# Kernel tuning notes

Hardware: AMD Instinct MI355X
Metric: run time of the kernel (lower is better)

## Reference

```python
import jax, jax.numpy as jnp
import numpy as np

TOP_K = 8
COAL_THR = 0.7

def _sign(x):
    s = jnp.sign(x)
    return jnp.where(s == 0, 1.0, s)

def setup_inputs() -> dict:
    key = jax.random.key(0)
    ks = jax.random.split(key, 12)
    B, N, D, P, H, NC = 4, 4096, 256, 64, 1024, 256
    def lin(k, fi, fo):
        return jax.random.normal(k, (fi, fo), dtype=jnp.float32) / np.sqrt(fi).astype(np.float32)
    return {
        "agent_states": jax.random.normal(ks[0], (B, N, D), dtype=jnp.float32),
        "agent_actions": jax.random.normal(ks[1], (B, N, D), dtype=jnp.float32),
        "episodic_mem": jax.random.normal(ks[2], (B, N, H), dtype=jnp.float32),
        "Wq": lin(ks[3], D, P), "bq": jnp.zeros((P,), jnp.float32),
        "Wk": lin(ks[4], D, P), "bk": jnp.zeros((P,), jnp.float32),
        "Wc": lin(ks[5], D, P), "bc": jnp.zeros((P,), jnp.float32),
        "Wh": lin(ks[6], D, H), "bh": jnp.zeros((H,), jnp.float32),
        "agent_keys": _sign(jax.random.normal(ks[7], (N, H), dtype=jnp.float32)),
        "pos_codes": _sign(jax.random.normal(ks[8], (NC, H), dtype=jnp.float32)),
        "step": 3,
    }

def reference(agent_states, agent_actions, episodic_mem,
              Wq, bq, Wk, bk, Wc, bc, Wh, bh, agent_keys, pos_codes, step):
    B, N, D = agent_states.shape
    P = Wq.shape[1]
    scale = jnp.asarray(np.sqrt(P), agent_states.dtype)

    # --- DynamicGraph.compute_graph(agent_actions) ---
    Q = agent_actions @ Wq + bq                       # (B,N,P)
    K = agent_actions @ Wk + bk                       # (B,N,P)
    scores = jnp.einsum('bnp,bmp->bnm', Q, K) / scale  # (B,N,N)
    _, ti = jax.lax.top_k(scores, TOP_K)               # (B,N,TOP_K)
    flat = scores.reshape(-1, N)
    rows = jnp.arange(flat.shape[0])[:, None]
    mask = jnp.zeros_like(flat).at[rows, ti.reshape(-1, TOP_K)].set(1.0).reshape(scores.shape)
    masked = scores * mask + (1.0 - mask) * (-1e9)
    adjacency = jax.nn.softmax(masked, axis=-1)        # (B,N,N)

    # message passing: each agent perceives a top-k mix of neighbor states
    incoming = jnp.einsum('bnm,bmd->bnd', adjacency, agent_states)  # (B,N,D)

    # --- AgentCombination(incoming, agent_actions) ---
    proj = agent_actions @ Wc + bc                    # (B,N,P)
    pn = proj / jnp.maximum(jnp.linalg.norm(proj, axis=-1, keepdims=True), 1e-12)
    sim = jnp.einsum('bnp,bmp->bnm', pn, pn)           # (B,N,N)
    cmask = (sim > COAL_THR).astype(proj.dtype)
    cw = cmask / (jnp.sum(cmask, axis=-1, keepdims=True) + 1e-8)
    combined = jnp.einsum('bnm,bmd->bnd', cw, incoming)
    out_states = 0.8 * incoming + 0.2 * combined      # (B,N,D)

    # --- HDCMemory: to_hdc -> bind agent key -> write(position) -> read ---
    hdc = jnp.tanh(3.0 * (out_states @ Wh + bh))       # (B,N,H) soft-bipolar
    personal = hdc * agent_keys[None]                  # bind with per-agent key
    pos = pos_codes[step % pos_codes.shape[0]]         # (H,)
    bound = personal * pos                             # bind with position code
    new_episodic = 0.95 * episodic_mem + 0.05 * bound  # write with decay
    # read: torch-style cosine similarity (norms clamped at 1e-8)
    na = jnp.maximum(jnp.linalg.norm(new_episodic, axis=-1), 1e-8)
    nb = jnp.maximum(jnp.linalg.norm(personal, axis=-1), 1e-8)
    mem_sim = jnp.sum(new_episodic * personal, axis=-1) / (na * nb)  # (B,N)

    return out_states, new_episodic, mem_sim
```

## Files before the change

### kernel.cpp

```cpp
#include <hip/hip_runtime.h>

#define BB 4
#define NN 4096
#define DD 256
#define PP 64
#define HH 1024
#define NCC 256
#define TOPK 8
#define CAP2 128

typedef __attribute__((ext_vector_type(8))) short s8v;
typedef __attribute__((ext_vector_type(4))) float f4v;

__device__ __forceinline__ void gload_lds16b(const unsigned short* g, unsigned short* l) {
    __builtin_amdgcn_global_load_lds(
        (const __attribute__((address_space(1))) void*)g,
        (__attribute__((address_space(3))) void*)l, 16, 0, 0);
}
__device__ __forceinline__ unsigned short f2b(float f) {
    unsigned int u = __float_as_uint(f);
    unsigned int r = (u + 0x7FFFu + ((u >> 16) & 1u)) >> 16;
    return (unsigned short)r;
}

__global__ __launch_bounds__(64) void k_gram(const float* __restrict__ Wk,
                                             float* __restrict__ G)
{
    int i = blockIdx.x, j = threadIdx.x;
    float s = 0.f;
#pragma unroll 8
    for (int d = 0; d < DD; ++d)
        s = fmaf(Wk[d * PP + i], Wk[d * PP + j], s);
    G[i * PP + j] = s;
}

__global__ __launch_bounds__(256) void k_proj(
    const float* __restrict__ act,
    const float* __restrict__ Wq, const float* __restrict__ bq,
    const float* __restrict__ Wk, const float* __restrict__ bk,
    const float* __restrict__ Wc, const float* __restrict__ bc,
    const float* __restrict__ Wh, const float* __restrict__ G,
    float* __restrict__ Qo, float* __restrict__ Ko,
    unsigned short* __restrict__ PNb, unsigned short* __restrict__ Whb,
    unsigned short* __restrict__ Kbo, float* __restrict__ Tg)
{
    __shared__ float As[16][DD];
    __shared__ float Ps[16][PP];
    const int tid = threadIdx.x;
    const long row0 = (long)blockIdx.x * 16;

    {
        const float4* g4 = (const float4*)(act + row0 * DD);
        float4* s4 = (float4*)(&As[0][0]);
#pragma unroll
        for (int i = 0; i < 4; ++i) s4[tid + i * 256] = g4[tid + i * 256];
    }
    {
        int h = blockIdx.x;
        Whb[(long)h * DD + tid] = f2b(Wh[(long)tid * HH + h]);
    }
    __syncthreads();

    const int col = tid & 63;
    const int rg  = tid >> 6;
    float aq[4], ak[4], ac[4];
#pragma unroll
    for (int j = 0; j < 4; ++j) { aq[j] = bq[col]; ak[j] = bk[col]; ac[j] = bc[col]; }

    for (int d = 0; d < DD; ++d) {
        float wq = Wq[d * PP + col];
        float wk = Wk[d * PP + col];
        float wc = Wc[d * PP + col];
#pragma unroll
        for (int j = 0; j < 4; ++j) {
            float a = As[rg * 4 + j][d];
            aq[j] = fmaf(a, wq, aq[j]);
            ak[j] = fmaf(a, wk, ak[j]);
            ac[j] = fmaf(a, wc, ac[j]);
        }
    }
    __syncthreads();

#pragma unroll
    for (int j = 0; j < 4; ++j) {
        long r = row0 + rg * 4 + j;
        Qo[r * PP + col] = aq[j];
        Ko[r * PP + col] = ak[j];
        Kbo[r * PP + col] = f2b(ak[j]);
        Ps[rg * 4 + j][col] = ac[j];
        As[rg * 4 + j][col] = aq[j];
    }
    __syncthreads();

    const int w = tid >> 6;
    const int lane = tid & 63;
#pragma unroll
    for (int j = 0; j < 4; ++j) {
        int r = w * 4 + j;
        float v = Ps[r][lane];
        float ss = v * v;
#pragma unroll
        for (int off = 32; off >= 1; off >>= 1) ss += __shfl_xor(ss, off, 64);
        float nrm = fmaxf(sqrtf(ss), 1e-12f);
        PNb[(row0 + r) * PP + lane] = f2b(v / nrm);
    }

#pragma unroll
    for (int j = 0; j < 4; ++j) {
        int r = w * 4 + j;
        float qc = As[r][lane];
        float gq = 0.f;
#pragma unroll 8
        for (int c2 = 0; c2 < 64; ++c2)
            gq = fmaf(G[c2 * PP + lane], As[r][c2], gq);
        float s2 = qc * gq;
        float mu = qc * bk[lane];
#pragma unroll
        for (int off = 32; off >= 1; off >>= 1) {
            s2 += __shfl_xor(s2, off, 64);
            mu += __shfl_xor(mu, off, 64);
        }
        if (lane == 0)
            Tg[row0 + r] = mu + 2.25f * sqrtf(fmaxf(s2, 0.f));
    }
}

__global__ __launch_bounds__(512, 8) void k_topk(
    const float* __restrict__ Q, const float* __restrict__ K,
    const unsigned short* __restrict__ Kb, const float* __restrict__ Tg,
    const float* __restrict__ states, float* __restrict__ incoming)
{
    __shared__ float Qsf[32][64];
    __shared__ unsigned short Bsb[2][128 * 64];
    __shared__ int cnt[32];
    __shared__ unsigned short lst[32][CAP2];
    __shared__ float scr[32][CAP2];

    const int tid = threadIdx.x;
    const int lane = tid & 63;
    const int wid = tid >> 6;
    const int obid = ((blockIdx.x & 7) << 6) | (blockIdx.x >> 3);
    const int b  = obid >> 7;
    const int n0 = (obid & 127) << 5;
    const int r = lane & 15, g = lane >> 4;

    if (tid < 32) cnt[tid] = 0;
    ((float4*)&Qsf[0][0])[tid] = ((const float4*)(Q + ((long)b * NN + n0) * PP))[tid];

    const unsigned short* KbB = Kb + (long)b * NN * PP;
    {
#pragma unroll
        for (int t = 0; t < 2; ++t) {
            int q = t * 512 + tid;
            int row = q >> 3, c = q & 7;
            int cs = c ^ (row & 7);
            gload_lds16b(KbB + row * PP + cs * 8,
                         &Bsb[0][0] + (t * 512 + wid * 64) * 8);
        }
    }
    __syncthreads();

    s8v afr[2][2];
#pragma unroll
    for (int j = 0; j < 2; ++j)
#pragma unroll
        for (int s = 0; s < 2; ++s) {
            int c = s * 4 + g;
            float4 x0 = *(const float4*)(&Qsf[j * 16 + r][c * 8]);
            float4 x1 = *(const float4*)(&Qsf[j * 16 + r][c * 8 + 4]);
            s8v h;
            h[0] = (short)f2b(x0.x); h[1] = (short)f2b(x0.y);
            h[2] = (short)f2b(x0.z); h[3] = (short)f2b(x0.w);
            h[4] = (short)f2b(x1.x); h[5] = (short)f2b(x1.y);
            h[6] = (short)f2b(x1.z); h[7] = (short)f2b(x1.w);
            afr[j][s] = h;
        }
    float tT[2][4];
#pragma unroll
    for (int j = 0; j < 2; ++j)
#pragma unroll
        for (int rr2 = 0; rr2 < 4; ++rr2)
            tT[j][rr2] = Tg[(long)b * NN + n0 + j * 16 + g * 4 + rr2];

    int cur = 0;
    for (int mt = 0; mt < NN / 128; ++mt) {
        if (mt + 1 < NN / 128) {
            const unsigned short* kb = KbB + (long)((mt + 1) << 7) * PP;
#pragma unroll
            for (int t = 0; t < 2; ++t) {
                int q = t * 512 + tid;
                int row = q >> 3, c = q & 7;
                int cs = c ^ (row & 7);
                gload_lds16b(kb + row * PP + cs * 8,
                             &Bsb[cur ^ 1][0] + (t * 512 + wid * 64) * 8);
            }
        }

        {
            const int m0 = mt << 7;
            const int mloc = wid * 16 + r;
            s8v bfr[2];
#pragma unroll
            for (int s = 0; s < 2; ++s) {
                int cd = (s * 4 + g) ^ (mloc & 7);
                bfr[s] = *(const s8v*)(&Bsb[cur][0] + mloc * 64 + cd * 8);
            }
#pragma unroll
            for (int j = 0; j < 2; ++j) {
                f4v acc = {0.f, 0.f, 0.f, 0.f};
#pragma unroll
                for (int s = 0; s < 2; ++s)
                    acc = __builtin_amdgcn_mfma_f32_16x16x32_bf16(afr[j][s], bfr[s], acc, 0, 0, 0);
#pragma unroll
                for (int rr2 = 0; rr2 < 4; ++rr2) {
                    if (acc[rr2] >= tT[j][rr2]) {
                        int qrow = j * 16 + g * 4 + rr2;
                        int pos = atomicAdd(&cnt[qrow], 1);
                        if (pos < CAP2)
                            lst[qrow][pos] = (unsigned short)(m0 + wid * 16 + r);
                    }
                }
            }
        }
        __syncthreads();
        cur ^= 1;
    }

    const int g16 = lane >> 4, li = lane & 15;
    const float4* K4all = (const float4*)(K + (long)b * NN * PP);
    for (int rr = wid * 4; rr < wid * 4 + 4; ++rr) {
        int c = cnt[rr]; if (c > CAP2) c = CAP2;

        float4 q4 = *(const float4*)(&Qsf[rr][li * 4]);
        for (int cd = g16; cd < c; cd += 4) {
            int idx = lst[rr][cd];
            float4 kv = K4all[(long)idx * 16 + li];
            float p = q4.x * kv.x;
            p = fmaf(q4.y, kv.y, p);
            p = fmaf(q4.z, kv.z, p);
            p = fmaf(q4.w, kv.w, p);
            p += __shfl_xor(p, 1, 64); p += __shfl_xor(p, 2, 64);
            p += __shfl_xor(p, 4, 64); p += __shfl_xor(p, 8, 64);
            if (li == 0) scr[rr][cd] = p;
        }

        float sc0 = -1e30f, sc1 = -1e30f;
        int i0 = 0x7FFFFFFF, i1 = 0x7FFFFFFF;
        if (lane < c)      { i0 = lst[rr][lane];      sc0 = scr[rr][lane]; }
        if (lane + 64 < c) { i1 = lst[rr][lane + 64]; sc1 = scr[rr][lane + 64]; }

        float wv[TOPK]; int wi[TOPK];
#pragma unroll
        for (int e = 0; e < TOPK; ++e) {
            bool p0 = (sc0 > sc1) || (sc0 == sc1 && i0 < i1);
            float lv = p0 ? sc0 : sc1;
            int   li2 = p0 ? i0 : i1;
#pragma unroll
            for (int off = 32; off >= 1; off >>= 1) {
                float ov = __shfl_xor(lv, off, 64);
                int   oi = __shfl_xor(li2, off, 64);
                bool tk = (ov > lv) || (ov == lv && oi < li2);
                lv = tk ? ov : lv;
                li2 = tk ? oi : li2;
            }
            wv[e] = lv; wi[e] = li2;
            if (sc0 == lv && i0 == li2)      { sc0 = -1e30f; i0 = 0x7FFFFFFF; }
            else if (sc1 == lv && i1 == li2) { sc1 = -1e30f; i1 = 0x7FFFFFFF; }
        }

        float mx = wv[0] * 0.125f;
        float ex[TOPK]; float Z = 0.f;
#pragma unroll
        for (int e = 0; e < TOPK; ++e) { ex[e] = expf(wv[e] * 0.125f - mx); Z += ex[e]; }
        float invZ = 1.0f / Z;

        float4 a0 = {0.f, 0.f, 0.f, 0.f};
#pragma unroll
        for (int e = 0; e < TOPK; ++e) {
            int gi = wi[e] & (NN - 1);
            float4 sv = ((const float4*)(states + ((long)b * NN + gi) * DD))[lane];
            float we = ex[e] * invZ;
            a0.x = fmaf(we, sv.x, a0.x); a0.y = fmaf(we, sv.y, a0.y);
            a0.z = fmaf(we, sv.z, a0.z); a0.w = fmaf(we, sv.w, a0.w);
        }
        ((float4*)(incoming + ((long)b * NN + n0 + rr) * DD))[lane] = a0;
    }
}

#define CAP 64
__global__ __launch_bounds__(256, 4) void k_coal(
    const unsigned short* __restrict__ PNb, const float* __restrict__ incoming,
    float* __restrict__ outs)
{
    __shared__ unsigned short Asb[16 * 64];
    __shared__ unsigned short Bsb[2][128 * 64];
    __shared__ int cnt[16];
    __shared__ unsigned short lst[16][CAP];

    const int tid = threadIdx.x;
    const int lane = tid & 63;
    const int wid = tid >> 6;
    const int obid = ((blockIdx.x & 7) << 7) | (blockIdx.x >> 3);
    const int b  = obid >> 8;
    const int n0 = (obid & 255) << 4;
    const int r = lane & 15, g = lane >> 4;

    if (tid < 16) cnt[tid] = 0;

    const unsigned short* PnB = PNb + (long)b * NN * PP;
    {
        const unsigned short* ab = PnB + (long)n0 * PP;
        if (tid < 128) {
            int row = tid >> 3, c = tid & 7;
            int cs = c ^ (row & 7);
            gload_lds16b(ab + row * PP + cs * 8, Asb + (wid * 64) * 8);
        }
    }
    {
#pragma unroll
        for (int t = 0; t < 4; ++t) {
            int q = t * 256 + tid;
            int row = q >> 3, c = q & 7;
            int cs = c ^ (row & 7);
            gload_lds16b(PnB + row * PP + cs * 8,
                         &Bsb[0][0] + (t * 256 + wid * 64) * 8);
        }
    }
    __syncthreads();

    s8v afr[2];
#pragma unroll
    for (int s = 0; s < 2; ++s) {
        int c = s * 4 + g;
        int cd = c ^ (r & 7);
        afr[s] = *(const s8v*)(Asb + r * 64 + cd * 8);
    }

    int cur = 0;
    for (int mt = 0; mt < NN / 128; ++mt) {
        if (mt + 1 < NN / 128) {
            const unsigned short* bb = PnB + (long)((mt + 1) << 7) * PP;
#pragma unroll
            for (int t = 0; t < 4; ++t) {
                int q = t * 256 + tid;
                int row = q >> 3, c = q & 7;
                int cs = c ^ (row & 7);
                gload_lds16b(bb + row * PP + cs * 8,
                             &Bsb[cur ^ 1][0] + (t * 256 + wid * 64) * 8);
            }
        }

        const int m0 = mt << 7;
#pragma unroll
        for (int t = 0; t < 2; ++t) {
            const int mrow = (wid * 2 + t) * 16 + r;
            f4v acc = {0.f, 0.f, 0.f, 0.f};
#pragma unroll
            for (int s = 0; s < 2; ++s) {
                int c = s * 4 + g;
                int cd = c ^ (mrow & 7);
                s8v bfr = *(const s8v*)(&Bsb[cur][0] + mrow * 64 + cd * 8);
                acc = __builtin_amdgcn_mfma_f32_16x16x32_bf16(afr[s], bfr, acc, 0, 0, 0);
            }
#pragma unroll
            for (int rr2 = 0; rr2 < 4; ++rr2) {
                if (acc[rr2] > 0.7f) {
                    int qrow = g * 4 + rr2;
                    int m = m0 + (wid * 2 + t) * 16 + r;
                    int pos = atomicAdd(&cnt[qrow], 1);
                    if (pos < CAP) lst[qrow][pos] = (unsigned short)m;
                }
            }
        }
        __syncthreads();
        cur ^= 1;
    }

    const int w = tid >> 6;
    for (int rr = w * 4; rr < w * 4 + 4; ++rr) {
        int c = cnt[rr];
        float inv = 1.0f / ((float)c + 1e-8f);
        int cc = (c < CAP) ? c : CAP;
        float ax = 0.f, ay = 0.f, az = 0.f, aw = 0.f;
        for (int i = 0; i < cc; ++i) {
            const float4* ip = (const float4*)(incoming + ((long)b * NN + lst[rr][i]) * DD);
            float4 v = ip[lane];
            ax += v.x; ay += v.y; az += v.z; aw += v.w;
        }
        const float4* self4 = (const float4*)(incoming + ((long)b * NN + n0 + rr) * DD);
        float4 sv = self4[lane];
        float4 o;
        o.x = 0.8f * sv.x + 0.2f * inv * ax;
        o.y = 0.8f * sv.y + 0.2f * inv * ay;
        o.z = 0.8f * sv.z + 0.2f * inv * az;
        o.w = 0.8f * sv.w + 0.2f * inv * aw;
        ((float4*)(outs + ((long)b * NN + n0 + rr) * DD))[lane] = o;
    }
}

__global__ __launch_bounds__(512, 4) void k_mem(
    const float* __restrict__ outs, const unsigned short* __restrict__ Whb,
    const float* __restrict__ bh, const float* __restrict__ keys,
    const float* __restrict__ pos_codes, const int* __restrict__ stepp,
    const float* __restrict__ mem,
    float* __restrict__ epi_out, float* __restrict__ sim_out)
{
    __shared__ unsigned short Ab[32 * 256];
    __shared__ unsigned short Bb[256 * 64];
    __shared__ float red[8][32][3];

    const int tid = threadIdx.x;
    const int lane = tid & 63;
    const int wid = tid >> 6;
    const long row0 = (long)blockIdx.x * 32;
    const int r = lane & 15, g = lane >> 4;

#pragma unroll
    for (int it = 0; it < 2; ++it) {
        int q = it * 512 + tid;
        int row = q >> 5, c = q & 31;
        const float4* src = (const float4*)(outs + (row0 + row) * DD + c * 8);
        float4 x0 = src[0], x1 = src[1];
        s8v h8;
        h8[0] = (short)f2b(x0.x); h8[1] = (short)f2b(x0.y);
        h8[2] = (short)f2b(x0.z); h8[3] = (short)f2b(x0.w);
        h8[4] = (short)f2b(x1.x); h8[5] = (short)f2b(x1.y);
        h8[6] = (short)f2b(x1.z); h8[7] = (short)f2b(x1.w);
        int cd = c ^ (row & 7);
        *(s8v*)(Ab + row * 256 + cd * 8) = h8;
    }

    const int step = stepp[0];
    const int prow = ((step % NCC) + NCC) % NCC;
    float snp[2][4], snn[2][4], spp[2][4];
#pragma unroll
    for (int j = 0; j < 2; ++j)
#pragma unroll
        for (int rr2 = 0; rr2 < 4; ++rr2) { snp[j][rr2] = 0.f; snn[j][rr2] = 0.f; spp[j][rr2] = 0.f; }

    for (int qt = 0; qt < 4; ++qt) {
        f4v acc[2][2];
#pragma unroll
        for (int j = 0; j < 2; ++j)
#pragma unroll
            for (int t = 0; t < 2; ++t) acc[j][t] = (f4v){0.f, 0.f, 0.f, 0.f};

        for (int ks = 0; ks < 4; ++ks) {
            __syncthreads();
            {
#pragma unroll
                for (int t4 = 0; t4 < 4; ++t4) {
                    int q = t4 * 512 + tid;
                    int row = q >> 3, c = q & 7;
                    int cs = c ^ (row & 7);
                    gload_lds16b(Whb + (long)(qt * 256 + row) * DD + ks * 64 + cs * 8,
                                 Bb + (t4 * 512 + wid * 64) * 8);
                }
            }
            __syncthreads();

            s8v af[2][2];
#pragma unroll
            for (int j = 0; j < 2; ++j)
#pragma unroll
                for (int s = 0; s < 2; ++s) {
                    int cA = ks * 8 + s * 4 + g;
                    int rA = j * 16 + r;
                    int cd = cA ^ (rA & 7);
                    af[j][s] = *(const s8v*)(Ab + rA * 256 + cd * 8);
                }
#pragma unroll
            for (int t = 0; t < 2; ++t) {
                const int hloc = (wid * 2 + t) * 16 + r;
#pragma unroll
                for (int s = 0; s < 2; ++s) {
                    int cd = (s * 4 + g) ^ (hloc & 7);
                    s8v bf = *(const s8v*)(Bb + hloc * 64 + cd * 8);
                    acc[0][t] = __builtin_amdgcn_mfma_f32_16x16x32_bf16(af[0][s], bf, acc[0][t], 0, 0, 0);
                    acc[1][t] = __builtin_amdgcn_mfma_f32_16x16x32_bf16(af[1][s], bf, acc[1][t], 0, 0, 0);
                }
            }
        }

#pragma unroll
        for (int t = 0; t < 2; ++t) {
            int h = qt * 256 + (wid * 2 + t) * 16 + r;
            float ps = pos_codes[(long)prow * HH + h];
            float bb_ = bh[h];
#pragma unroll
            for (int j = 0; j < 2; ++j)
#pragma unroll
                for (int rr2 = 0; rr2 < 4; ++rr2) {
                    long row = row0 + j * 16 + g * 4 + rr2;
                    int n = (int)(row & (NN - 1));
                    float y = acc[j][t][rr2] + bb_;
                    float e = __expf(6.0f * y);
                    float hd = 1.0f - __fdividef(2.0f, e + 1.0f);
                    float pe = hd * keys[(long)n * HH + h];
                    float ne = 0.95f * mem[row * HH + h] + 0.05f * (pe * ps);
                    epi_out[row * HH + h] = ne;
                    snp[j][rr2] = fmaf(ne, pe, snp[j][rr2]);
                    snn[j][rr2] = fmaf(ne, ne, snn[j][rr2]);
                    spp[j][rr2] = fmaf(pe, pe, spp[j][rr2]);
                }
        }
    }

#pragma unroll
    for (int j = 0; j < 2; ++j)
#pragma unroll
        for (int rr2 = 0; rr2 < 4; ++rr2) {
#pragma unroll
            for (int off = 1; off <= 8; off <<= 1) {
                snp[j][rr2] += __shfl_xor(snp[j][rr2], off, 64);
                snn[j][rr2] += __shfl_xor(snn[j][rr2], off, 64);
                spp[j][rr2] += __shfl_xor(spp[j][rr2], off, 64);
            }
        }
    if (r == 0) {
#pragma unroll
        for (int j = 0; j < 2; ++j)
#pragma unroll
            for (int rr2 = 0; rr2 < 4; ++rr2) {
                int rw = j * 16 + g * 4 + rr2;
                red[wid][rw][0] = snp[j][rr2];
                red[wid][rw][1] = snn[j][rr2];
                red[wid][rw][2] = spp[j][rr2];
            }
    }
    __syncthreads();
    if (tid < 32) {
        float dot = 0.f, nn = 0.f, pp = 0.f;
#pragma unroll
        for (int wv = 0; wv < 8; ++wv) {
            dot += red[wv][tid][0]; nn += red[wv][tid][1]; pp += red[wv][tid][2];
        }
        float na = fmaxf(sqrtf(nn), 1e-8f);
        float nb = fmaxf(sqrtf(pp), 1e-8f);
        sim_out[row0 + tid] = dot / (na * nb);
    }
}

extern "C" void kernel_launch(void* const* d_in, const int* in_sizes, int n_in,
                              void* d_out, int out_size, void* d_ws, size_t ws_size,
                              hipStream_t stream)
{
    const float* states  = (const float*)d_in[0];
    const float* actions = (const float*)d_in[1];
    const float* mem     = (const float*)d_in[2];
    const float* Wq = (const float*)d_in[3];
    const float* bq = (const float*)d_in[4];
    const float* Wk = (const float*)d_in[5];
    const float* bk = (const float*)d_in[6];
    const float* Wc = (const float*)d_in[7];
    const float* bc = (const float*)d_in[8];
    const float* Wh = (const float*)d_in[9];
    const float* bh = (const float*)d_in[10];
    const float* keys = (const float*)d_in[11];
    const float* pos  = (const float*)d_in[12];
    const int*   step = (const int*)d_in[13];

    float* ws = (float*)d_ws;
    float* Q        = ws;
    float* K        = ws + 1048576;
    unsigned short* PNb = (unsigned short*)(ws + 2097152);
    unsigned short* Whb = PNb + 1048576;
    float* incoming = ws + 3145728;
    unsigned short* Kb = (unsigned short*)(ws + 7340032);
    float* Tg       = ws + 7340032 + 524288;
    float* G        = Tg + 16384;

    float* outs = (float*)d_out;
    float* epi  = outs + (long)BB * NN * DD;
    float* simo = epi + (long)BB * NN * HH;

    hipLaunchKernelGGL(k_gram, dim3(64), dim3(64), 0, stream, Wk, G);
    hipLaunchKernelGGL(k_proj, dim3(BB * NN / 16), dim3(256), 0, stream,
                       actions, Wq, bq, Wk, bk, Wc, bc, Wh, G,
                       Q, K, PNb, Whb, Kb, Tg);
    hipLaunchKernelGGL(k_topk, dim3(BB * (NN / 32)), dim3(512), 0, stream,
                       Q, K, Kb, Tg, states, incoming);
    hipLaunchKernelGGL(k_coal, dim3(BB * (NN / 16)), dim3(256), 0, stream,
                       PNb, incoming, outs);
    hipLaunchKernelGGL(k_mem, dim3(BB * NN / 32), dim3(512), 0, stream,
                       outs, Whb, bh, keys, pos, step, mem, epi, simo);
}
```

Measured before the change: 212.4 us.

## Split top-k kernel into candidate collection and per-row final selection kernels

The fused top-k kernel is split in two. The first kernel does the bf16 MFMA candidate filtering and writes each row's candidate list and count into the incoming buffer as scratch. A second kernel, one wave per row, rescoring candidates in fp32, selects the top-8, applies the softmax and gathers states. The aim is to free LDS in the heavy MFMA kernel for higher occupancy and to spread the serial per-row tail across many small blocks. The cost is an extra launch and a global round trip for the candidate lists.

```diff
diff --git a/kernel.cpp b/kernel.cpp
--- a/kernel.cpp
+++ b/kernel.cpp
@@ -125,16 +125,15 @@
     }
 }
 
-__global__ __launch_bounds__(512, 8) void k_topk(
-    const float* __restrict__ Q, const float* __restrict__ K,
+__global__ __launch_bounds__(512, 8) void k_collect(
+    const float* __restrict__ Q,
     const unsigned short* __restrict__ Kb, const float* __restrict__ Tg,
-    const float* __restrict__ states, float* __restrict__ incoming)
+    float* __restrict__ incoming)
 {
     __shared__ float Qsf[32][64];
     __shared__ unsigned short Bsb[2][128 * 64];
     __shared__ int cnt[32];
     __shared__ unsigned short lst[32][CAP2];
-    __shared__ float scr[32][CAP2];
 
     const int tid = threadIdx.x;
     const int lane = tid & 63;
@@ -195,7 +194,6 @@
                              &Bsb[cur ^ 1][0] + (t * 512 + wid * 64) * 8);
             }
         }
-
         {
             const int m0 = mt << 7;
             const int mloc = wid * 16 + r;
@@ -226,65 +224,87 @@
         cur ^= 1;
     }
 
+    float* ibase = incoming + ((long)b * NN + n0) * DD;
+    if (tid < 32) *(int*)(ibase + (long)tid * DD + 64) = cnt[tid];
+    for (int k = tid; k < 32 * 64; k += 512) {
+        int rr = k >> 6, off = k & 63;
+        ((unsigned int*)(ibase + (long)rr * DD))[off] = ((unsigned int*)&lst[rr][0])[off];
+    }
+}
+
+__global__ __launch_bounds__(256, 8) void k_final(
+    const float* __restrict__ Q, const float* __restrict__ K,
+    const float* __restrict__ states, float* __restrict__ incoming)
+{
+    __shared__ float scr[4][CAP2];
+
+    const int tid = threadIdx.x;
+    const int lane = tid & 63;
+    const int wid = tid >> 6;
+    const long row = (long)blockIdx.x * 4 + wid;
+    const int b = (int)(row >> 12);
+    const int n = (int)(row & (NN - 1));
     const int g16 = lane >> 4, li = lane & 15;
+
+    float* irow = incoming + row * DD;
+    int c = *(const int*)(irow + 64);
+    if (c > CAP2) c = CAP2;
+    const unsigned short* lrow = (const unsigned short*)irow;
+
     const float4* K4all = (const float4*)(K + (long)b * NN * PP);
-    for (int rr = wid * 4; rr < wid * 4 + 4; ++rr) {
-        int c = cnt[rr]; if (c > CAP2) c = CAP2;
-
-        float4 q4 = *(const float4*)(&Qsf[rr][li * 4]);
-        for (int cd = g16; cd < c; cd += 4) {
-            int idx = lst[rr][cd];
-            float4 kv = K4all[(long)idx * 16 + li];
-            float p = q4.x * kv.x;
-            p = fmaf(q4.y, kv.y, p);
-            p = fmaf(q4.z, kv.z, p);
-            p = fmaf(q4.w, kv.w, p);
-            p += __shfl_xor(p, 1, 64); p += __shfl_xor(p, 2, 64);
-            p += __shfl_xor(p, 4, 64); p += __shfl_xor(p, 8, 64);
-            if (li == 0) scr[rr][cd] = p;
-        }
-
-        float sc0 = -1e30f, sc1 = -1e30f;
-        int i0 = 0x7FFFFFFF, i1 = 0x7FFFFFFF;
-        if (lane < c)      { i0 = lst[rr][lane];      sc0 = scr[rr][lane]; }
-        if (lane + 64 < c) { i1 = lst[rr][lane + 64]; sc1 = scr[rr][lane + 64]; }
-
-        float wv[TOPK]; int wi[TOPK];
-#pragma unroll
-        for (int e = 0; e < TOPK; ++e) {
-            bool p0 = (sc0 > sc1) || (sc0 == sc1 && i0 < i1);
-            float lv = p0 ? sc0 : sc1;
-            int   li2 = p0 ? i0 : i1;
-#pragma unroll
-            for (int off = 32; off >= 1; off >>= 1) {
-                float ov = __shfl_xor(lv, off, 64);
-                int   oi = __shfl_xor(li2, off, 64);
-                bool tk = (ov > lv) || (ov == lv && oi < li2);
-                lv = tk ? ov : lv;
-                li2 = tk ? oi : li2;
-            }
-            wv[e] = lv; wi[e] = li2;
-            if (sc0 == lv && i0 == li2)      { sc0 = -1e30f; i0 = 0x7FFFFFFF; }
-            else if (sc1 == lv && i1 == li2) { sc1 = -1e30f; i1 = 0x7FFFFFFF; }
-        }
-
-        float mx = wv[0] * 0.125f;
-        float ex[TOPK]; float Z = 0.f;
-#pragma unroll
-        for (int e = 0; e < TOPK; ++e) { ex[e] = expf(wv[e] * 0.125f - mx); Z += ex[e]; }
-        float invZ = 1.0f / Z;
-
-        float4 a0 = {0.f, 0.f, 0.f, 0.f};
-#pragma unroll
-        for (int e = 0; e < TOPK; ++e) {
-            int gi = wi[e] & (NN - 1);
-            float4 sv = ((const float4*)(states + ((long)b * NN + gi) * DD))[lane];
-            float we = ex[e] * invZ;
-            a0.x = fmaf(we, sv.x, a0.x); a0.y = fmaf(we, sv.y, a0.y);
-            a0.z = fmaf(we, sv.z, a0.z); a0.w = fmaf(we, sv.w, a0.w);
-        }
-        ((float4*)(incoming + ((long)b * NN + n0 + rr) * DD))[lane] = a0;
-    }
+    float4 q4 = ((const float4*)(Q + ((long)b * NN + n) * PP))[li];
+    for (int cd = g16; cd < c; cd += 4) {
+        int idx = lrow[cd];
+        float4 kv = K4all[(long)idx * 16 + li];
+        float p = q4.x * kv.x;
+        p = fmaf(q4.y, kv.y, p);
+        p = fmaf(q4.z, kv.z, p);
+        p = fmaf(q4.w, kv.w, p);
+        p += __shfl_xor(p, 1, 64); p += __shfl_xor(p, 2, 64);
+        p += __shfl_xor(p, 4, 64); p += __shfl_xor(p, 8, 64);
+        if (li == 0) scr[wid][cd] = p;
+    }
+
+    float sc0 = -1e30f, sc1 = -1e30f;
+    int i0 = 0x7FFFFFFF, i1 = 0x7FFFFFFF;
+    if (lane < c)      { i0 = lrow[lane];      sc0 = scr[wid][lane]; }
+    if (lane + 64 < c) { i1 = lrow[lane + 64]; sc1 = scr[wid][lane + 64]; }
+
+    float wv[TOPK]; int wi[TOPK];
+#pragma unroll
+    for (int e = 0; e < TOPK; ++e) {
+        bool p0 = (sc0 > sc1) || (sc0 == sc1 && i0 < i1);
+        float lv = p0 ? sc0 : sc1;
+        int   li2 = p0 ? i0 : i1;
+#pragma unroll
+        for (int off = 32; off >= 1; off >>= 1) {
+            float ov = __shfl_xor(lv, off, 64);
+            int   oi = __shfl_xor(li2, off, 64);
+            bool tk = (ov > lv) || (ov == lv && oi < li2);
+            lv = tk ? ov : lv;
+            li2 = tk ? oi : li2;
+        }
+        wv[e] = lv; wi[e] = li2;
+        if (sc0 == lv && i0 == li2)      { sc0 = -1e30f; i0 = 0x7FFFFFFF; }
+        else if (sc1 == lv && i1 == li2) { sc1 = -1e30f; i1 = 0x7FFFFFFF; }
+    }
+
+    float mx = wv[0] * 0.125f;
+    float ex[TOPK]; float Z = 0.f;
+#pragma unroll
+    for (int e = 0; e < TOPK; ++e) { ex[e] = expf(wv[e] * 0.125f - mx); Z += ex[e]; }
+    float invZ = 1.0f / Z;
+
+    float4 a0 = {0.f, 0.f, 0.f, 0.f};
+#pragma unroll
+    for (int e = 0; e < TOPK; ++e) {
+        int gi = wi[e] & (NN - 1);
+        float4 sv = ((const float4*)(states + ((long)b * NN + gi) * DD))[lane];
+        float we = ex[e] * invZ;
+        a0.x = fmaf(we, sv.x, a0.x); a0.y = fmaf(we, sv.y, a0.y);
+        a0.z = fmaf(we, sv.z, a0.z); a0.w = fmaf(we, sv.w, a0.w);
+    }
+    ((float4*)irow)[lane] = a0;
 }
 
 #define CAP 64
@@ -578,8 +598,10 @@
     hipLaunchKernelGGL(k_proj, dim3(BB * NN / 16), dim3(256), 0, stream,
                        actions, Wq, bq, Wk, bk, Wc, bc, Wh, G,
                        Q, K, PNb, Whb, Kb, Tg);
-    hipLaunchKernelGGL(k_topk, dim3(BB * (NN / 32)), dim3(512), 0, stream,
-                       Q, K, Kb, Tg, states, incoming);
+    hipLaunchKernelGGL(k_collect, dim3(BB * (NN / 32)), dim3(512), 0, stream,
+                       Q, Kb, Tg, incoming);
+    hipLaunchKernelGGL(k_final, dim3(BB * NN / 4), dim3(256), 0, stream,
+                       Q, K, states, incoming);
     hipLaunchKernelGGL(k_coal, dim3(BB * (NN / 16)), dim3(256), 0, stream,
                        PNb, incoming, outs);
     hipLaunchKernelGGL(k_mem, dim3(BB * NN / 32), dim3(512), 0, stream,
```

Result: no change. 213.7 us (median of 3 runs) (+0.6%).
